# Kernel optimization log

Measured on AMD Instinct MI355X. Metric: run time of the kernel, lower is better.

## Reference

```python
import jax, jax.numpy as jnp
import numpy as np
import math

B, S, H, D = 1, 4096, 16, 64
SM_SCALE = 1.0 / math.sqrt(D)

def setup_inputs() -> dict:
    key = jax.random.key(0)
    kq, kk, kv = jax.random.split(key, 3)
    return {
        "query": jax.random.normal(kq, (B, S, H, D), dtype=jnp.float32),
        "key": jax.random.normal(kk, (B, S, H, D), dtype=jnp.float32),
        "value": jax.random.normal(kv, (B, S, H, D), dtype=jnp.float32),
    }

def reference(query, key, value):
    # Module transposes [B,S,H,D] -> [B,H,S,D]; S=4096 is already a multiple of
    # 128 so padding / segment-id masking is a no-op. Backend is non-causal
    # flash attention with sm_scale = 1/sqrt(D); equivalent dense math:
    # scores: [B,H,Sq,Sk]
    scores = jnp.einsum("bqhd,bkhd->bhqk", query, key) * SM_SCALE
    probs = jax.nn.softmax(scores, axis=-1)
    out = jnp.einsum("bhqk,bkhd->bqhd", probs, value)
    return out  # [B,S,H,D]
```

## Files before the change

kernel.cpp:

```cpp
#include <hip/hip_runtime.h>
#include <stdint.h>

#define H_ 16
#define S_ 4096
#define D_ 64
#define ROWSTRIDE (H_ * D_)
#define BK 64
#define NT (S_ / BK)
#define TILE_USH (BK * D_)
#define NBUF 4
#define BUF_USH (2 * TILE_USH)
#define LP 72
#define LK 72
#define QSCALE (0.125f * 1.44269504088896340736f)
#define LOG2E 1.44269504088896340736f
#define SM_SCALE 0.125f

typedef unsigned short ushort_t;
typedef __attribute__((ext_vector_type(8))) __bf16 bf16x8;
typedef __attribute__((ext_vector_type(16))) float floatx16;
typedef __attribute__((ext_vector_type(8))) unsigned short ushortx8;
typedef __attribute__((ext_vector_type(4))) unsigned short ushortx4;

#if __has_builtin(__builtin_amdgcn_exp2f)
#define EXP2F(x) __builtin_amdgcn_exp2f(x)
#else
#define EXP2F(x) exp2f(x)
#endif

__device__ inline unsigned short f2bf(float x) {
    union { float f; unsigned int u; } c; c.f = x;
    unsigned int r = c.u + 0x7fffu + ((c.u >> 16) & 1u);
    return (unsigned short)(r >> 16);
}
__device__ inline uint32_t cvt_pk_bf16(float a, float b) {
#if __has_builtin(__builtin_amdgcn_cvt_pk_bf16_f32)
    auto r = __builtin_amdgcn_cvt_pk_bf16_f32(a, b);
    uint32_t u; __builtin_memcpy(&u, &r, 4); return u;
#else
    return (uint32_t)f2bf(a) | ((uint32_t)f2bf(b) << 16);
#endif
}
__device__ inline void permswap(uint32_t& a, uint32_t& b, int g2) {
#if __has_builtin(__builtin_amdgcn_permlane32_swap)
    auto r = __builtin_amdgcn_permlane32_swap(a, b, false, false);
    uint32_t tmp[2]; __builtin_memcpy(tmp, &r, 8);
    a = tmp[0]; b = tmp[1];
#else
    uint32_t ra = (uint32_t)__shfl_xor((int)a, 32, 64);
    uint32_t rb = (uint32_t)__shfl_xor((int)b, 32, 64);
    uint32_t na = g2 ? rb : a;
    uint32_t nb = g2 ? b : ra;
    a = na; b = nb;
#endif
}
__device__ inline bf16x8 as_bf16x8(ushortx8 v) {
    union { ushortx8 s; bf16x8 b; } c; c.s = v; return c.b;
}
__device__ inline bf16x8 bf16x8_from_u32(uint32_t a, uint32_t b, uint32_t c, uint32_t d) {
    union { uint32_t u[4]; bf16x8 b; } x; x.u[0]=a; x.u[1]=b; x.u[2]=c; x.u[3]=d; return x.b;
}
__device__ inline void glds16(const void* g, void* l) {
    __builtin_amdgcn_global_load_lds(
        (const __attribute__((address_space(1))) void*)g,
        (__attribute__((address_space(3))) void*)l, 16, 0, 0);
}

__global__ __launch_bounds__(256)
void pack_kv(const float* __restrict__ K, const float* __restrict__ V,
             ushort_t* __restrict__ Kp, ushort_t* __restrict__ Vp) {
    __shared__ ushort_t lT[D_ * 88];
    const int tid = threadIdx.x;
    const int h = blockIdx.x & (H_ - 1);
    const int tile = blockIdx.x >> 4;
    ushort_t* kout = Kp + (size_t)(h * NT + tile) * TILE_USH;
    ushort_t* vout = Vp + (size_t)(h * NT + tile) * TILE_USH;
    #pragma unroll
    for (int p = 0; p < 4; ++p) {
        int idx = tid + p * 256;
        int row = idx >> 4;
        int d4 = (idx & 15) * 4;
        const float* kp = K + (size_t)(tile * BK + row) * ROWSTRIDE + h * D_ + d4;
        float4 kv = *(const float4*)kp;
        ushortx4 ku;
        ku[0] = f2bf(kv.x); ku[1] = f2bf(kv.y); ku[2] = f2bf(kv.z); ku[3] = f2bf(kv.w);
        *(ushortx4*)&kout[row * 64 + (((d4 >> 3) ^ (row & 7)) * 8) + (d4 & 7)] = ku;
        const float* vp = V + (size_t)(tile * BK + row) * ROWSTRIDE + h * D_ + d4;
        float4 vv = *(const float4*)vp;
        lT[(d4 + 0) * 88 + row] = f2bf(vv.x);
        lT[(d4 + 1) * 88 + row] = f2bf(vv.y);
        lT[(d4 + 2) * 88 + row] = f2bf(vv.z);
        lT[(d4 + 3) * 88 + row] = f2bf(vv.w);
    }
    __syncthreads();
    #pragma unroll
    for (int p = 0; p < 2; ++p) {
        int cid = tid + p * 256;
        int rowd = cid >> 3;
        int j = cid & 7;
        ushortx8 val = *(ushortx8*)&lT[rowd * 88 + j * 8];
        *(ushortx8*)&vout[rowd * 64 + ((j ^ (rowd & 7)) * 8)] = val;
    }
}

__global__ __launch_bounds__(320)
void usp_attn_fa6(const float* __restrict__ Q, const ushort_t* __restrict__ Kp,
                  const ushort_t* __restrict__ Vp, float* __restrict__ O) {
    __shared__ __attribute__((aligned(16))) ushort_t smem[NBUF * BUF_USH];
    __shared__ int flags[8];

    const int tid = threadIdx.x;
    const int lane = tid & 63;
    const int wv = tid >> 6;
    const int h = blockIdx.x & (H_ - 1);
    const int qi = blockIdx.x >> 4;
    const int l31 = lane & 31;
    const int g2 = lane >> 5;

    if (tid < 8) flags[tid] = 0;
    __syncthreads();

    const ushort_t* kbase = Kp + (size_t)h * NT * TILE_USH;
    const ushort_t* vbase = Vp + (size_t)h * NT * TILE_USH;

    if (wv == 4) {
        for (int t = 0; t < NT; ++t) {
            if (t >= NBUF) {
                for (;;) {
                    int m0 = __hip_atomic_load(&flags[4], __ATOMIC_ACQUIRE, __HIP_MEMORY_SCOPE_WORKGROUP);
                    int m1 = __hip_atomic_load(&flags[5], __ATOMIC_ACQUIRE, __HIP_MEMORY_SCOPE_WORKGROUP);
                    int m2 = __hip_atomic_load(&flags[6], __ATOMIC_ACQUIRE, __HIP_MEMORY_SCOPE_WORKGROUP);
                    int m3 = __hip_atomic_load(&flags[7], __ATOMIC_ACQUIRE, __HIP_MEMORY_SCOPE_WORKGROUP);
                    int m = min(min(m0, m1), min(m2, m3));
                    if (m >= t - (NBUF - 1)) break;
                    __builtin_amdgcn_s_sleep(1);
                }
            }
            const ushort_t* gK = kbase + (size_t)t * TILE_USH;
            const ushort_t* gV = vbase + (size_t)t * TILE_USH;
            ushort_t* bK = smem + (t & (NBUF - 1)) * BUF_USH;
            ushort_t* bV = bK + TILE_USH;
            #pragma unroll
            for (int i = 0; i < 8; ++i) {
                glds16(gK + i * 512 + lane * 8, bK + i * 512);
                glds16(gV + i * 512 + lane * 8, bV + i * 512);
            }
            __builtin_amdgcn_s_waitcnt(0x0f70);
            __hip_atomic_store(&flags[0], t + 1, __ATOMIC_RELEASE, __HIP_MEMORY_SCOPE_WORKGROUP);
        }
        return;
    }

    const int q0 = qi * 128 + wv * 32;

    bf16x8 qf[4];
    {
        const float* qp = Q + (size_t)(q0 + l31) * ROWSTRIDE + h * D_ + g2 * 8;
        #pragma unroll
        for (int c = 0; c < 4; ++c) {
            const float4 v0 = *(const float4*)(qp + c * 16);
            const float4 v1 = *(const float4*)(qp + c * 16 + 4);
            qf[c] = bf16x8_from_u32(
                cvt_pk_bf16(v0.x * QSCALE, v0.y * QSCALE),
                cvt_pk_bf16(v0.z * QSCALE, v0.w * QSCALE),
                cvt_pk_bf16(v1.x * QSCALE, v1.y * QSCALE),
                cvt_pk_bf16(v1.z * QSCALE, v1.w * QSCALE));
        }
    }

    floatx16 o[2] = {{0,0,0,0,0,0,0,0,0,0,0,0,0,0,0,0},
                     {0,0,0,0,0,0,0,0,0,0,0,0,0,0,0,0}};
    float rs = 0.f;

    for (int t = 0; t < NT; ++t) {
        while (__hip_atomic_load(&flags[0], __ATOMIC_ACQUIRE, __HIP_MEMORY_SCOPE_WORKGROUP) < t + 1)
            __builtin_amdgcn_s_sleep(1);
        const ushort_t* tK  = smem + (t & (NBUF - 1)) * BUF_USH;
        const ushort_t* tVT = tK + TILE_USH;

        floatx16 st[2];
        #pragma unroll
        for (int mk = 0; mk < 2; ++mk) {
            floatx16 acc = {0,0,0,0,0,0,0,0,0,0,0,0,0,0,0,0};
            int row = mk * 32 + l31;
            int sx = row & 7;
            #pragma unroll
            for (int c = 0; c < 4; ++c) {
                bf16x8 kf = as_bf16x8(*(const ushortx8*)&tK[row * 64 + (((2 * c + g2) ^ sx) * 8)]);
                acc = __builtin_amdgcn_mfma_f32_32x32x16_bf16(kf, qf[c], acc, 0, 0, 0);
            }
            st[mk] = acc;
        }

        uint32_t qd[2][8];
        #pragma unroll
        for (int mk = 0; mk < 2; ++mk) {
            #pragma unroll
            for (int i = 0; i < 8; ++i) {
                float p0 = EXP2F(st[mk][2 * i]);
                float p1 = EXP2F(st[mk][2 * i + 1]);
                rs += p0 + p1;
                qd[mk][i] = cvt_pk_bf16(p0, p1);
            }
        }

        #pragma unroll
        for (int kc = 0; kc < 4; ++kc) {
            int mk = kc >> 1, ci = kc & 1;
            uint32_t a0 = qd[mk][ci * 4 + 0], a1 = qd[mk][ci * 4 + 1];
            uint32_t b0 = qd[mk][ci * 4 + 2], b1 = qd[mk][ci * 4 + 3];
            permswap(a0, b0, g2);
            permswap(a1, b1, g2);
            bf16x8 pf = bf16x8_from_u32(a0, a1, b0, b1);
            #pragma unroll
            for (int md = 0; md < 2; ++md) {
                int row = md * 32 + l31;
                bf16x8 vf = as_bf16x8(*(const ushortx8*)&tVT[row * 64 + (((2 * kc + g2) ^ (row & 7)) * 8)]);
                o[md] = __builtin_amdgcn_mfma_f32_32x32x16_bf16(vf, pf, o[md], 0, 0, 0);
            }
        }

        __hip_atomic_store(&flags[4 + wv], t + 1, __ATOMIC_RELEASE, __HIP_MEMORY_SCOPE_WORKGROUP);
    }

    rs += __shfl_xor(rs, 32, 64);
    float inv = 1.f / rs;
    float* op = O + (size_t)(q0 + l31) * ROWSTRIDE + h * D_;
    #pragma unroll
    for (int md = 0; md < 2; ++md) {
        #pragma unroll
        for (int rq = 0; rq < 4; ++rq) {
            int d0 = md * 32 + rq * 8 + 4 * g2;
            float4 w;
            w.x = o[md][4 * rq + 0] * inv;
            w.y = o[md][4 * rq + 1] * inv;
            w.z = o[md][4 * rq + 2] * inv;
            w.w = o[md][4 * rq + 3] * inv;
            *(float4*)&op[d0] = w;
        }
    }
}

__global__ __launch_bounds__(256, 2)
void usp_attn_fa(const float* __restrict__ Q, const float* __restrict__ K,
                 const float* __restrict__ V, float* __restrict__ O) {
    __shared__ unsigned short fK[BK * LK];
    __shared__ unsigned short fVT[D_ * LK];
    __shared__ unsigned short fP[4 * 16 * LP];
    const int tid = threadIdx.x;
    const int lane = tid & 63;
    const int wv = tid >> 6;
    const int h = blockIdx.x & (H_ - 1);
    const int qt = blockIdx.x >> 4;
    const int q0 = qt * 64 + wv * 16;
    const int m16 = lane & 15;
    const int g = lane >> 4;
    typedef __attribute__((ext_vector_type(4))) float f4;
    bf16x8 qf[2];
    {
        const float* qp = Q + (size_t)(q0 + m16) * ROWSTRIDE + h * D_ + g * 8;
        for (int c = 0; c < 2; ++c) {
            ushortx8 u;
            #pragma unroll
            for (int j = 0; j < 8; ++j) u[j] = f2bf(qp[c * 32 + j]);
            qf[c] = as_bf16x8(u);
        }
    }
    f4 o[4] = {{0,0,0,0},{0,0,0,0},{0,0,0,0},{0,0,0,0}};
    float mrow[4] = {-1e30f,-1e30f,-1e30f,-1e30f};
    float lrow[4] = {0.f,0.f,0.f,0.f};
    unsigned short* myP = &fP[wv * 16 * LP];
    for (int k0 = 0; k0 < S_; k0 += BK) {
        __syncthreads();
        #pragma unroll
        for (int p = 0; p < 4; ++p) {
            int idx = tid + p * 256;
            int row = idx >> 4;
            int c4 = (idx & 15) * 4;
            const float* kp = K + (size_t)(k0 + row) * ROWSTRIDE + h * D_ + c4;
            float4 kv = *(const float4*)kp;
            ushortx4 ku;
            ku[0] = f2bf(kv.x); ku[1] = f2bf(kv.y); ku[2] = f2bf(kv.z); ku[3] = f2bf(kv.w);
            *(ushortx4*)&fK[row * LK + c4] = ku;
            const float* vp = V + (size_t)(k0 + row) * ROWSTRIDE + h * D_ + c4;
            float4 vv = *(const float4*)vp;
            fVT[(c4 + 0) * LK + row] = f2bf(vv.x);
            fVT[(c4 + 1) * LK + row] = f2bf(vv.y);
            fVT[(c4 + 2) * LK + row] = f2bf(vv.z);
            fVT[(c4 + 3) * LK + row] = f2bf(vv.w);
        }
        __syncthreads();
        f4 s[4];
        #pragma unroll
        for (int t = 0; t < 4; ++t) {
            f4 acc = {0,0,0,0};
            #pragma unroll
            for (int c = 0; c < 2; ++c) {
                bf16x8 kf = as_bf16x8(*(ushortx8*)&fK[(t * 16 + m16) * LK + c * 32 + g * 8]);
                acc = __builtin_amdgcn_mfma_f32_16x16x32_bf16(qf[c], kf, acc, 0, 0, 0);
            }
            s[t] = acc * SM_SCALE;
        }
        float mnew[4], rsum[4];
        #pragma unroll
        for (int r = 0; r < 4; ++r) {
            float pm = fmaxf(fmaxf(s[0][r], s[1][r]), fmaxf(s[2][r], s[3][r]));
            #pragma unroll
            for (int msk = 1; msk <= 8; msk <<= 1) pm = fmaxf(pm, __shfl_xor(pm, msk, 64));
            mnew[r] = fmaxf(mrow[r], pm);
            rsum[r] = 0.f;
        }
        #pragma unroll
        for (int t = 0; t < 4; ++t) {
            #pragma unroll
            for (int r = 0; r < 4; ++r) {
                float p = EXP2F((s[t][r] - mnew[r]) * LOG2E);
                rsum[r] += p;
                myP[(g * 4 + r) * LP + t * 16 + m16] = f2bf(p);
            }
        }
        #pragma unroll
        for (int r = 0; r < 4; ++r) {
            #pragma unroll
            for (int msk = 1; msk <= 8; msk <<= 1) rsum[r] += __shfl_xor(rsum[r], msk, 64);
            float alpha = EXP2F((mrow[r] - mnew[r]) * LOG2E);
            lrow[r] = lrow[r] * alpha + rsum[r];
            mrow[r] = mnew[r];
            o[0][r] *= alpha; o[1][r] *= alpha; o[2][r] *= alpha; o[3][r] *= alpha;
        }
        #pragma unroll
        for (int c = 0; c < 2; ++c) {
            bf16x8 pf = as_bf16x8(*(ushortx8*)&myP[m16 * LP + c * 32 + g * 8]);
            #pragma unroll
            for (int t = 0; t < 4; ++t) {
                bf16x8 vf = as_bf16x8(*(ushortx8*)&fVT[(t * 16 + m16) * LK + c * 32 + g * 8]);
                o[t] = __builtin_amdgcn_mfma_f32_16x16x32_bf16(pf, vf, o[t], 0, 0, 0);
            }
        }
    }
    float* op = O + (size_t)q0 * ROWSTRIDE + h * D_;
    #pragma unroll
    for (int r = 0; r < 4; ++r) {
        float inv = 1.f / lrow[r];
        int row = g * 4 + r;
        #pragma unroll
        for (int t = 0; t < 4; ++t)
            op[(size_t)row * ROWSTRIDE + t * 16 + m16] = o[t][r] * inv;
    }
}

extern "C" void kernel_launch(void* const* d_in, const int* in_sizes, int n_in,
                              void* d_out, int out_size, void* d_ws, size_t ws_size,
                              hipStream_t stream) {
    const float* Q = (const float*)d_in[0];
    const float* K = (const float*)d_in[1];
    const float* V = (const float*)d_in[2];
    float* O = (float*)d_out;
    const size_t packed = (size_t)H_ * NT * TILE_USH;
    const size_t packed_bytes = 2 * packed * sizeof(ushort_t);
    if (ws_size >= packed_bytes) {
        ushort_t* Kp = (ushort_t*)d_ws;
        ushort_t* Vp = Kp + packed;
        pack_kv<<<dim3(H_ * NT), dim3(256), 0, stream>>>(K, V, Kp, Vp);
        usp_attn_fa6<<<dim3(H_ * (S_ / 128)), dim3(320), 0, stream>>>(Q, Kp, Vp, O);
    } else {
        usp_attn_fa<<<dim3(H_ * (S_ / 64)), dim3(256), 0, stream>>>(Q, K, V, O);
    }
}
```

Before: 189.1 us.

## Pack K/V in MFMA fragment order and give each wave 64 query rows

The pack kernel now writes K and transposed V tiles in exact per-lane MFMA fragment order, so the attention kernel reads each operand as a contiguous 16-byte vector per lane with no swizzle arithmetic. The attention block shrinks to two compute waves plus one loader wave, with each compute wave handling two 32-row query slices. Each K/V fragment loaded from LDS is reused across both slices, halving LDS reads per query row. The cost is more registers per wave (16 K/V fragments plus doubled accumulators) and fewer waves per block to hide latency, which could reduce occupancy.

```diff
diff --git a/kernel.cpp b/kernel.cpp
--- a/kernel.cpp
+++ b/kernel.cpp
@@ -75,16 +75,28 @@
     const int tile = blockIdx.x >> 4;
     ushort_t* kout = Kp + (size_t)(h * NT + tile) * TILE_USH;
     ushort_t* vout = Vp + (size_t)(h * NT + tile) * TILE_USH;
+
+    #pragma unroll
+    for (int p = 0; p < 2; ++p) {
+        int idx = tid + p * 256;
+        int f = idx >> 6;
+        int lo = idx & 63;
+        int mk = f >> 2, c = f & 3;
+        int l31 = lo & 31, g2 = lo >> 5;
+        const float* kp = K + (size_t)(tile * BK + mk * 32 + l31) * ROWSTRIDE + h * D_ + (2 * c + g2) * 8;
+        float4 a = *(const float4*)kp;
+        float4 b = *(const float4*)(kp + 4);
+        ushortx8 u;
+        u[0] = f2bf(a.x); u[1] = f2bf(a.y); u[2] = f2bf(a.z); u[3] = f2bf(a.w);
+        u[4] = f2bf(b.x); u[5] = f2bf(b.y); u[6] = f2bf(b.z); u[7] = f2bf(b.w);
+        *(ushortx8*)&kout[f * 512 + lo * 8] = u;
+    }
+
     #pragma unroll
     for (int p = 0; p < 4; ++p) {
         int idx = tid + p * 256;
         int row = idx >> 4;
         int d4 = (idx & 15) * 4;
-        const float* kp = K + (size_t)(tile * BK + row) * ROWSTRIDE + h * D_ + d4;
-        float4 kv = *(const float4*)kp;
-        ushortx4 ku;
-        ku[0] = f2bf(kv.x); ku[1] = f2bf(kv.y); ku[2] = f2bf(kv.z); ku[3] = f2bf(kv.w);
-        *(ushortx4*)&kout[row * 64 + (((d4 >> 3) ^ (row & 7)) * 8) + (d4 & 7)] = ku;
         const float* vp = V + (size_t)(tile * BK + row) * ROWSTRIDE + h * D_ + d4;
         float4 vv = *(const float4*)vp;
         lT[(d4 + 0) * 88 + row] = f2bf(vv.x);
@@ -95,16 +107,18 @@
     __syncthreads();
     #pragma unroll
     for (int p = 0; p < 2; ++p) {
-        int cid = tid + p * 256;
-        int rowd = cid >> 3;
-        int j = cid & 7;
-        ushortx8 val = *(ushortx8*)&lT[rowd * 88 + j * 8];
-        *(ushortx8*)&vout[rowd * 64 + ((j ^ (rowd & 7)) * 8)] = val;
-    }
-}
-
-__global__ __launch_bounds__(320)
-void usp_attn_fa6(const float* __restrict__ Q, const ushort_t* __restrict__ Kp,
+        int idx = tid + p * 256;
+        int f = idx >> 6;
+        int lo = idx & 63;
+        int md = f >> 2, kc = f & 3;
+        int l31 = lo & 31, g2 = lo >> 5;
+        ushortx8 u = *(ushortx8*)&lT[(md * 32 + l31) * 88 + (2 * kc + g2) * 8];
+        *(ushortx8*)&vout[f * 512 + lo * 8] = u;
+    }
+}
+
+__global__ __launch_bounds__(192)
+void usp_attn_fa7(const float* __restrict__ Q, const ushort_t* __restrict__ Kp,
                   const ushort_t* __restrict__ Vp, float* __restrict__ O) {
     __shared__ __attribute__((aligned(16))) ushort_t smem[NBUF * BUF_USH];
     __shared__ int flags[8];
@@ -123,16 +137,13 @@
     const ushort_t* kbase = Kp + (size_t)h * NT * TILE_USH;
     const ushort_t* vbase = Vp + (size_t)h * NT * TILE_USH;
 
-    if (wv == 4) {
+    if (wv == 2) {
         for (int t = 0; t < NT; ++t) {
             if (t >= NBUF) {
                 for (;;) {
                     int m0 = __hip_atomic_load(&flags[4], __ATOMIC_ACQUIRE, __HIP_MEMORY_SCOPE_WORKGROUP);
                     int m1 = __hip_atomic_load(&flags[5], __ATOMIC_ACQUIRE, __HIP_MEMORY_SCOPE_WORKGROUP);
-                    int m2 = __hip_atomic_load(&flags[6], __ATOMIC_ACQUIRE, __HIP_MEMORY_SCOPE_WORKGROUP);
-                    int m3 = __hip_atomic_load(&flags[7], __ATOMIC_ACQUIRE, __HIP_MEMORY_SCOPE_WORKGROUP);
-                    int m = min(min(m0, m1), min(m2, m3));
-                    if (m >= t - (NBUF - 1)) break;
+                    if (min(m0, m1) >= t - (NBUF - 1)) break;
                     __builtin_amdgcn_s_sleep(1);
                 }
             }
@@ -151,16 +162,17 @@
         return;
     }
 
-    const int q0 = qi * 128 + wv * 32;
-
-    bf16x8 qf[4];
-    {
-        const float* qp = Q + (size_t)(q0 + l31) * ROWSTRIDE + h * D_ + g2 * 8;
+    const int q0 = qi * 128 + wv * 64;
+
+    bf16x8 qf[2][4];
+    #pragma unroll
+    for (int qs = 0; qs < 2; ++qs) {
+        const float* qp = Q + (size_t)(q0 + qs * 32 + l31) * ROWSTRIDE + h * D_ + g2 * 8;
         #pragma unroll
         for (int c = 0; c < 4; ++c) {
             const float4 v0 = *(const float4*)(qp + c * 16);
             const float4 v1 = *(const float4*)(qp + c * 16 + 4);
-            qf[c] = bf16x8_from_u32(
+            qf[qs][c] = bf16x8_from_u32(
                 cvt_pk_bf16(v0.x * QSCALE, v0.y * QSCALE),
                 cvt_pk_bf16(v0.z * QSCALE, v0.w * QSCALE),
                 cvt_pk_bf16(v1.x * QSCALE, v1.y * QSCALE),
@@ -168,75 +180,80 @@
         }
     }
 
-    floatx16 o[2] = {{0,0,0,0,0,0,0,0,0,0,0,0,0,0,0,0},
-                     {0,0,0,0,0,0,0,0,0,0,0,0,0,0,0,0}};
-    float rs = 0.f;
+    floatx16 o[2][2] = {{{0,0,0,0,0,0,0,0,0,0,0,0,0,0,0,0},
+                         {0,0,0,0,0,0,0,0,0,0,0,0,0,0,0,0}},
+                        {{0,0,0,0,0,0,0,0,0,0,0,0,0,0,0,0},
+                         {0,0,0,0,0,0,0,0,0,0,0,0,0,0,0,0}}};
+    float rs[2] = {0.f, 0.f};
 
     for (int t = 0; t < NT; ++t) {
         while (__hip_atomic_load(&flags[0], __ATOMIC_ACQUIRE, __HIP_MEMORY_SCOPE_WORKGROUP) < t + 1)
             __builtin_amdgcn_s_sleep(1);
-        const ushort_t* tK  = smem + (t & (NBUF - 1)) * BUF_USH;
-        const ushort_t* tVT = tK + TILE_USH;
-
-        floatx16 st[2];
-        #pragma unroll
-        for (int mk = 0; mk < 2; ++mk) {
-            floatx16 acc = {0,0,0,0,0,0,0,0,0,0,0,0,0,0,0,0};
-            int row = mk * 32 + l31;
-            int sx = row & 7;
-            #pragma unroll
-            for (int c = 0; c < 4; ++c) {
-                bf16x8 kf = as_bf16x8(*(const ushortx8*)&tK[row * 64 + (((2 * c + g2) ^ sx) * 8)]);
-                acc = __builtin_amdgcn_mfma_f32_32x32x16_bf16(kf, qf[c], acc, 0, 0, 0);
-            }
-            st[mk] = acc;
-        }
-
-        uint32_t qd[2][8];
-        #pragma unroll
-        for (int mk = 0; mk < 2; ++mk) {
-            #pragma unroll
-            for (int i = 0; i < 8; ++i) {
-                float p0 = EXP2F(st[mk][2 * i]);
-                float p1 = EXP2F(st[mk][2 * i + 1]);
-                rs += p0 + p1;
-                qd[mk][i] = cvt_pk_bf16(p0, p1);
-            }
-        }
-
-        #pragma unroll
-        for (int kc = 0; kc < 4; ++kc) {
-            int mk = kc >> 1, ci = kc & 1;
-            uint32_t a0 = qd[mk][ci * 4 + 0], a1 = qd[mk][ci * 4 + 1];
-            uint32_t b0 = qd[mk][ci * 4 + 2], b1 = qd[mk][ci * 4 + 3];
-            permswap(a0, b0, g2);
-            permswap(a1, b1, g2);
-            bf16x8 pf = bf16x8_from_u32(a0, a1, b0, b1);
-            #pragma unroll
-            for (int md = 0; md < 2; ++md) {
-                int row = md * 32 + l31;
-                bf16x8 vf = as_bf16x8(*(const ushortx8*)&tVT[row * 64 + (((2 * kc + g2) ^ (row & 7)) * 8)]);
-                o[md] = __builtin_amdgcn_mfma_f32_32x32x16_bf16(vf, pf, o[md], 0, 0, 0);
+
+        const ushortx8* fp = (const ushortx8*)(smem + (t & (NBUF - 1)) * BUF_USH) + lane;
+        ushortx8 kfr[8], vfr[8];
+        #pragma unroll
+        for (int f = 0; f < 8; ++f) kfr[f] = fp[f * 64];
+        #pragma unroll
+        for (int f = 0; f < 8; ++f) vfr[f] = fp[512 + f * 64];
+
+        #pragma unroll
+        for (int qs = 0; qs < 2; ++qs) {
+            floatx16 st[2];
+            #pragma unroll
+            for (int mk = 0; mk < 2; ++mk) {
+                floatx16 acc = {0,0,0,0,0,0,0,0,0,0,0,0,0,0,0,0};
+                #pragma unroll
+                for (int c = 0; c < 4; ++c)
+                    acc = __builtin_amdgcn_mfma_f32_32x32x16_bf16(as_bf16x8(kfr[mk * 4 + c]), qf[qs][c], acc, 0, 0, 0);
+                st[mk] = acc;
+            }
+            uint32_t qd[2][8];
+            #pragma unroll
+            for (int mk = 0; mk < 2; ++mk) {
+                #pragma unroll
+                for (int i = 0; i < 8; ++i) {
+                    float p0 = EXP2F(st[mk][2 * i]);
+                    float p1 = EXP2F(st[mk][2 * i + 1]);
+                    rs[qs] += p0 + p1;
+                    qd[mk][i] = cvt_pk_bf16(p0, p1);
+                }
+            }
+            #pragma unroll
+            for (int kc = 0; kc < 4; ++kc) {
+                int mk = kc >> 1, ci = kc & 1;
+                uint32_t a0 = qd[mk][ci * 4 + 0], a1 = qd[mk][ci * 4 + 1];
+                uint32_t b0 = qd[mk][ci * 4 + 2], b1 = qd[mk][ci * 4 + 3];
+                permswap(a0, b0, g2);
+                permswap(a1, b1, g2);
+                bf16x8 pf = bf16x8_from_u32(a0, a1, b0, b1);
+                #pragma unroll
+                for (int md = 0; md < 2; ++md)
+                    o[qs][md] = __builtin_amdgcn_mfma_f32_32x32x16_bf16(as_bf16x8(vfr[md * 4 + kc]), pf, o[qs][md], 0, 0, 0);
             }
         }
 
         __hip_atomic_store(&flags[4 + wv], t + 1, __ATOMIC_RELEASE, __HIP_MEMORY_SCOPE_WORKGROUP);
     }
 
-    rs += __shfl_xor(rs, 32, 64);
-    float inv = 1.f / rs;
-    float* op = O + (size_t)(q0 + l31) * ROWSTRIDE + h * D_;
-    #pragma unroll
-    for (int md = 0; md < 2; ++md) {
-        #pragma unroll
-        for (int rq = 0; rq < 4; ++rq) {
-            int d0 = md * 32 + rq * 8 + 4 * g2;
-            float4 w;
-            w.x = o[md][4 * rq + 0] * inv;
-            w.y = o[md][4 * rq + 1] * inv;
-            w.z = o[md][4 * rq + 2] * inv;
-            w.w = o[md][4 * rq + 3] * inv;
-            *(float4*)&op[d0] = w;
+    #pragma unroll
+    for (int qs = 0; qs < 2; ++qs) {
+        float v = rs[qs];
+        v += __shfl_xor(v, 32, 64);
+        float inv = 1.f / v;
+        float* op = O + (size_t)(q0 + qs * 32 + l31) * ROWSTRIDE + h * D_;
+        #pragma unroll
+        for (int md = 0; md < 2; ++md) {
+            #pragma unroll
+            for (int rq = 0; rq < 4; ++rq) {
+                int d0 = md * 32 + rq * 8 + 4 * g2;
+                float4 w;
+                w.x = o[qs][md][4 * rq + 0] * inv;
+                w.y = o[qs][md][4 * rq + 1] * inv;
+                w.z = o[qs][md][4 * rq + 2] * inv;
+                w.w = o[qs][md][4 * rq + 3] * inv;
+                *(float4*)&op[d0] = w;
+            }
         }
     }
 }
@@ -362,7 +379,7 @@
         ushort_t* Kp = (ushort_t*)d_ws;
         ushort_t* Vp = Kp + packed;
         pack_kv<<<dim3(H_ * NT), dim3(256), 0, stream>>>(K, V, Kp, Vp);
-        usp_attn_fa6<<<dim3(H_ * (S_ / 128)), dim3(320), 0, stream>>>(Q, Kp, Vp, O);
+        usp_attn_fa7<<<dim3(H_ * (S_ / 128)), dim3(192), 0, stream>>>(Q, Kp, Vp, O);
     } else {
         usp_attn_fa<<<dim3(H_ * (S_ / 64)), dim3(256), 0, stream>>>(Q, K, V, O);
     }
```

Result: slower. 236.4 us (+25.0%).

## Pack K/V tiles in MFMA fragment order and shrink LDS ring to two buffers

Applied to the files above, without the earlier changes.

The pack kernel now writes K and transposed V in the exact per-lane fragment order the MFMA loop consumes, so each lane reads a contiguous 16-byte chunk at lane*8 with a constant offset. This removes the per-load row/XOR swizzle address arithmetic in the inner loop and makes LDS reads linear. The LDS ring buffer also drops from four to two stages, which halves shared memory per block and may raise occupancy. The cost is a shallower prefetch depth, so the producer wave can stall more often waiting for consumers.

```diff
diff --git a/kernel.cpp b/kernel.cpp
--- a/kernel.cpp
+++ b/kernel.cpp
@@ -8,7 +8,7 @@
 #define BK 64
 #define NT (S_ / BK)
 #define TILE_USH (BK * D_)
-#define NBUF 4
+#define NBUF 2
 #define BUF_USH (2 * TILE_USH)
 #define LP 72
 #define LK 72
@@ -75,16 +75,28 @@
     const int tile = blockIdx.x >> 4;
     ushort_t* kout = Kp + (size_t)(h * NT + tile) * TILE_USH;
     ushort_t* vout = Vp + (size_t)(h * NT + tile) * TILE_USH;
+
+    #pragma unroll
+    for (int p = 0; p < 2; ++p) {
+        int idx = tid + p * 256;
+        int f = idx >> 6;
+        int lo = idx & 63;
+        int mk = f >> 2, c = f & 3;
+        int l31 = lo & 31, g2 = lo >> 5;
+        const float* kp = K + (size_t)(tile * BK + mk * 32 + l31) * ROWSTRIDE + h * D_ + (2 * c + g2) * 8;
+        float4 a = *(const float4*)kp;
+        float4 b = *(const float4*)(kp + 4);
+        ushortx8 u;
+        u[0] = f2bf(a.x); u[1] = f2bf(a.y); u[2] = f2bf(a.z); u[3] = f2bf(a.w);
+        u[4] = f2bf(b.x); u[5] = f2bf(b.y); u[6] = f2bf(b.z); u[7] = f2bf(b.w);
+        *(ushortx8*)&kout[f * 512 + lo * 8] = u;
+    }
+
     #pragma unroll
     for (int p = 0; p < 4; ++p) {
         int idx = tid + p * 256;
         int row = idx >> 4;
         int d4 = (idx & 15) * 4;
-        const float* kp = K + (size_t)(tile * BK + row) * ROWSTRIDE + h * D_ + d4;
-        float4 kv = *(const float4*)kp;
-        ushortx4 ku;
-        ku[0] = f2bf(kv.x); ku[1] = f2bf(kv.y); ku[2] = f2bf(kv.z); ku[3] = f2bf(kv.w);
-        *(ushortx4*)&kout[row * 64 + (((d4 >> 3) ^ (row & 7)) * 8) + (d4 & 7)] = ku;
         const float* vp = V + (size_t)(tile * BK + row) * ROWSTRIDE + h * D_ + d4;
         float4 vv = *(const float4*)vp;
         lT[(d4 + 0) * 88 + row] = f2bf(vv.x);
@@ -95,16 +107,18 @@
     __syncthreads();
     #pragma unroll
     for (int p = 0; p < 2; ++p) {
-        int cid = tid + p * 256;
-        int rowd = cid >> 3;
-        int j = cid & 7;
-        ushortx8 val = *(ushortx8*)&lT[rowd * 88 + j * 8];
-        *(ushortx8*)&vout[rowd * 64 + ((j ^ (rowd & 7)) * 8)] = val;
+        int idx = tid + p * 256;
+        int f = idx >> 6;
+        int lo = idx & 63;
+        int md = f >> 2, kc = f & 3;
+        int l31 = lo & 31, g2 = lo >> 5;
+        ushortx8 u = *(ushortx8*)&lT[(md * 32 + l31) * 88 + (2 * kc + g2) * 8];
+        *(ushortx8*)&vout[f * 512 + lo * 8] = u;
     }
 }
 
 __global__ __launch_bounds__(320)
-void usp_attn_fa6(const float* __restrict__ Q, const ushort_t* __restrict__ Kp,
+void usp_attn_fa8(const float* __restrict__ Q, const ushort_t* __restrict__ Kp,
                   const ushort_t* __restrict__ Vp, float* __restrict__ O) {
     __shared__ __attribute__((aligned(16))) ushort_t smem[NBUF * BUF_USH];
     __shared__ int flags[8];
@@ -131,8 +145,7 @@
                     int m1 = __hip_atomic_load(&flags[5], __ATOMIC_ACQUIRE, __HIP_MEMORY_SCOPE_WORKGROUP);
                     int m2 = __hip_atomic_load(&flags[6], __ATOMIC_ACQUIRE, __HIP_MEMORY_SCOPE_WORKGROUP);
                     int m3 = __hip_atomic_load(&flags[7], __ATOMIC_ACQUIRE, __HIP_MEMORY_SCOPE_WORKGROUP);
-                    int m = min(min(m0, m1), min(m2, m3));
-                    if (m >= t - (NBUF - 1)) break;
+                    if (min(min(m0, m1), min(m2, m3)) >= t - (NBUF - 1)) break;
                     __builtin_amdgcn_s_sleep(1);
                 }
             }
@@ -175,20 +188,15 @@
     for (int t = 0; t < NT; ++t) {
         while (__hip_atomic_load(&flags[0], __ATOMIC_ACQUIRE, __HIP_MEMORY_SCOPE_WORKGROUP) < t + 1)
             __builtin_amdgcn_s_sleep(1);
-        const ushort_t* tK  = smem + (t & (NBUF - 1)) * BUF_USH;
-        const ushort_t* tVT = tK + TILE_USH;
+        const ushortx8* fp = (const ushortx8*)(smem + (t & (NBUF - 1)) * BUF_USH) + lane;
 
         floatx16 st[2];
         #pragma unroll
         for (int mk = 0; mk < 2; ++mk) {
             floatx16 acc = {0,0,0,0,0,0,0,0,0,0,0,0,0,0,0,0};
-            int row = mk * 32 + l31;
-            int sx = row & 7;
-            #pragma unroll
-            for (int c = 0; c < 4; ++c) {
-                bf16x8 kf = as_bf16x8(*(const ushortx8*)&tK[row * 64 + (((2 * c + g2) ^ sx) * 8)]);
-                acc = __builtin_amdgcn_mfma_f32_32x32x16_bf16(kf, qf[c], acc, 0, 0, 0);
-            }
+            #pragma unroll
+            for (int c = 0; c < 4; ++c)
+                acc = __builtin_amdgcn_mfma_f32_32x32x16_bf16(as_bf16x8(fp[(mk * 4 + c) * 64]), qf[c], acc, 0, 0, 0);
             st[mk] = acc;
         }
 
@@ -213,11 +221,8 @@
             permswap(a1, b1, g2);
             bf16x8 pf = bf16x8_from_u32(a0, a1, b0, b1);
             #pragma unroll
-            for (int md = 0; md < 2; ++md) {
-                int row = md * 32 + l31;
-                bf16x8 vf = as_bf16x8(*(const ushortx8*)&tVT[row * 64 + (((2 * kc + g2) ^ (row & 7)) * 8)]);
-                o[md] = __builtin_amdgcn_mfma_f32_32x32x16_bf16(vf, pf, o[md], 0, 0, 0);
-            }
+            for (int md = 0; md < 2; ++md)
+                o[md] = __builtin_amdgcn_mfma_f32_32x32x16_bf16(as_bf16x8(fp[512 + (md * 4 + kc) * 64]), pf, o[md], 0, 0, 0);
         }
 
         __hip_atomic_store(&flags[4 + wv], t + 1, __ATOMIC_RELEASE, __HIP_MEMORY_SCOPE_WORKGROUP);
@@ -362,7 +367,7 @@
         ushort_t* Kp = (ushort_t*)d_ws;
         ushort_t* Vp = Kp + packed;
         pack_kv<<<dim3(H_ * NT), dim3(256), 0, stream>>>(K, V, Kp, Vp);
-        usp_attn_fa6<<<dim3(H_ * (S_ / 128)), dim3(320), 0, stream>>>(Q, Kp, Vp, O);
+        usp_attn_fa8<<<dim3(H_ * (S_ / 128)), dim3(320), 0, stream>>>(Q, Kp, Vp, O);
     } else {
         usp_attn_fa<<<dim3(H_ * (S_ / 64)), dim3(256), 0, stream>>>(Q, K, V, O);
     }
```

After: 188.1 us. Within noise of the previous version (-0.5%).
